# Optimization experiments

Measured on AMD Instinct MI355X. Metric: run time of the kernel, lower is better.

The kernel has to match this reference:

```python
import jax, jax.numpy as jnp
import numpy as np

N_EMBD = 1024
N_HEAD = 16
HEAD_DIM = N_EMBD // N_HEAD


def setup_inputs() -> dict:
    key = jax.random.key(0)
    ks = jax.random.split(key, 9)
    B, S = 4, 2048
    s = 1.0 / np.sqrt(N_EMBD)
    return {
        "x": jax.random.normal(ks[0], (B, S, N_EMBD), dtype=jnp.float32),
        "attention_mask": jnp.ones((B, S), dtype=jnp.int32),
        "Wq": jax.random.normal(ks[1], (N_EMBD, N_EMBD), jnp.float32) * s,
        "bq": jnp.zeros((N_EMBD,), jnp.float32),
        "Wk": jax.random.normal(ks[2], (N_EMBD, N_EMBD), jnp.float32) * s,
        "bk": jnp.zeros((N_EMBD,), jnp.float32),
        "Wv": jax.random.normal(ks[3], (N_EMBD, N_EMBD), jnp.float32) * s,
        "bv": jnp.zeros((N_EMBD,), jnp.float32),
        "Wo": jax.random.normal(ks[4], (N_EMBD, N_EMBD), jnp.float32) * s,
        "bo": jnp.zeros((N_EMBD,), jnp.float32),
    }


def _split_heads(t):  # [B,S,E] -> [B,H,S,D]
    B, S, _ = t.shape
    return t.reshape(B, S, N_HEAD, HEAD_DIM).transpose(0, 2, 1, 3)


def reference(x, attention_mask, Wq, bq, Wk, bk, Wv, bv, Wo, bo):
    B, S, E = x.shape
    q = _split_heads(x @ Wq.T + bq)
    k = _split_heads(x @ Wk.T + bk)
    v = _split_heads(x @ Wv.T + bv)
    # scores: [B,H,S,S]
    scores = jnp.einsum('bhqd,bhkd->bhqk', q, k) / np.sqrt(HEAD_DIM).astype(np.float32)
    # additive mask: 0 where mask==1, -inf where mask==0, broadcast over heads/query
    mask = jnp.where(attention_mask[:, None, None, :] == 0, -jnp.inf, 0.0).astype(scores.dtype)
    scores = scores + mask
    probs = jax.nn.softmax(scores, axis=-1)  # dropout p=0 -> identity
    ctx = jnp.einsum('bhqk,bhkd->bhqd', probs, v)
    out = ctx.transpose(0, 2, 1, 3).reshape(B, S, E)
    return out @ Wo.T + bo
```

## Files before the change

### kernel.cpp

```cpp
#include <hip/hip_runtime.h>

typedef __bf16 bf16;
typedef __attribute__((ext_vector_type(2))) bf16 bf16x2;
typedef __attribute__((ext_vector_type(4))) bf16 bf16x4;
typedef __attribute__((ext_vector_type(8))) bf16 bf16x8;
typedef __attribute__((ext_vector_type(4))) float f32x4;
typedef __attribute__((ext_vector_type(16))) float f32x16;
typedef __attribute__((ext_vector_type(4))) int i32x4;
typedef __attribute__((ext_vector_type(2))) int i32x2;

#define MFMA_BF16(a, b, c) __builtin_amdgcn_mfma_f32_16x16x32_bf16((a), (b), (c), 0, 0, 0)
#define MFMA32(a, b, c)    __builtin_amdgcn_mfma_f32_32x32x16_bf16((a), (b), (c), 0, 0, 0)

constexpr int S_LEN = 2048;
constexpr int EMB   = 1024;
constexpr int NHEAD = 16;
constexpr int HDIM  = 64;
constexpr int BATCH = 4;
constexpr int NTOK  = BATCH * S_LEN;

__device__ __forceinline__ void gload_lds16(const bf16* g, bf16* l) {
    __builtin_amdgcn_global_load_lds(
        (const __attribute__((address_space(1))) void*)g,
        (__attribute__((address_space(3))) void*)l, 16, 0, 0);
}

__device__ __forceinline__ int pkbf(float a, float b) {
    bf16x2 t; t[0] = (bf16)a; t[1] = (bf16)b;
    return __builtin_bit_cast(int, t);
}

#if __has_builtin(__builtin_amdgcn_permlane32_swap)
__device__ __forceinline__ i32x2 permswap(int a, int b) {
    return __builtin_amdgcn_permlane32_swap(a, b, false, false);
}
#else
__device__ __forceinline__ i32x2 permswap(int a, int b) {
    int as = __shfl_xor(a, 32);
    int bs = __shfl_xor(b, 32);
    int hx_ = (threadIdx.x >> 5) & 1;
    i32x2 r;
    r[0] = hx_ ? bs : a;
    r[1] = hx_ ? b : as;
    return r;
}
#endif

__global__ __launch_bounds__(256)
void cvt_f32_bf16(const float* __restrict__ src, bf16* __restrict__ dst, int n4) {
    int i = blockIdx.x * 256 + threadIdx.x;
    if (i < n4) {
        f32x4 v = ((const f32x4*)src)[i];
        bf16x4 o;
        o[0] = (bf16)v[0]; o[1] = (bf16)v[1]; o[2] = (bf16)v[2]; o[3] = (bf16)v[3];
        ((bf16x4*)dst)[i] = o;
    }
}

__global__ __launch_bounds__(256)
void gemm_bt(const bf16* __restrict__ A,
             const bf16* __restrict__ W0, const bf16* __restrict__ W1, const bf16* __restrict__ W2,
             const float* __restrict__ b0, const float* __restrict__ b1, const float* __restrict__ b2,
             void* __restrict__ d0, void* __restrict__ d1, void* __restrict__ d2,
             int fused, float q_scale)
{
    __shared__ bf16 al[128 * 32];
    __shared__ bf16 bl[128 * 32];

    int seg, mode, n0;
    if (fused) { seg = blockIdx.y >> 3; n0 = (blockIdx.y & 7) * 128; mode = (seg == 2) ? 1 : 0; }
    else       { seg = 0;              n0 = blockIdx.y * 128;        mode = 2; }
    const bf16*  W    = seg == 0 ? W0 : (seg == 1 ? W1 : W2);
    const float* bias = seg == 0 ? b0 : (seg == 1 ? b1 : b2);
    void*        C    = seg == 0 ? d0 : (seg == 1 ? d1 : d2);
    const float  osc  = (fused && seg == 0) ? q_scale : 1.0f;

    const int tid  = threadIdx.x;
    const int lane = tid & 63;
    const int w    = tid >> 6;
    const int quad = lane >> 4;
    const int l16  = lane & 15;
    const int wm   = (w >> 1) * 64;
    const int wn   = (w & 1) * 64;
    const int m0   = blockIdx.x * 128;

    f32x4 acc[4][4] = {};

    for (int k0 = 0; k0 < EMB; k0 += 32) {
        #pragma unroll
        for (int c = 0; c < 2; ++c) {
            int idx = c * 256 + tid;
            int row = idx >> 2, kc = idx & 3;
            gload_lds16(A + (size_t)(m0 + row) * EMB + k0 + kc * 8, &al[idx * 8]);
            gload_lds16(W + (size_t)(n0 + row) * EMB + k0 + kc * 8, &bl[idx * 8]);
        }
        __syncthreads();

        bf16x8 afrag[4], bfrag[4];
        #pragma unroll
        for (int t = 0; t < 4; ++t)
            afrag[t] = *(const bf16x8*)&al[(wm + t * 16 + l16) * 32 + quad * 8];
        #pragma unroll
        for (int t = 0; t < 4; ++t)
            bfrag[t] = *(const bf16x8*)&bl[(wn + t * 16 + l16) * 32 + quad * 8];

        #pragma unroll
        for (int mt = 0; mt < 4; ++mt)
            #pragma unroll
            for (int nt = 0; nt < 4; ++nt)
                acc[mt][nt] = MFMA_BF16(afrag[mt], bfrag[nt], acc[mt][nt]);

        __syncthreads();
    }

    #pragma unroll
    for (int mt = 0; mt < 4; ++mt) {
        #pragma unroll
        for (int nt = 0; nt < 4; ++nt) {
            int col = n0 + wn + nt * 16 + l16;
            float bv = bias[col];
            int row0 = m0 + wm + mt * 16 + quad * 4;
            if (mode == 1) {
                int bb = row0 >> 11, s0 = row0 & 2047;
                int hh = col >> 6,   d  = col & 63;
                bf16x4 pk;
                #pragma unroll
                for (int r = 0; r < 4; ++r) pk[r] = (bf16)(acc[mt][nt][r] + bv);
                *(bf16x4*)((bf16*)C + (size_t)((bb * NHEAD + hh) * HDIM + d) * S_LEN + s0) = pk;
            } else if (mode == 0) {
                #pragma unroll
                for (int r = 0; r < 4; ++r)
                    ((bf16*)C)[(size_t)(row0 + r) * EMB + col] = (bf16)((acc[mt][nt][r] + bv) * osc);
            } else {
                #pragma unroll
                for (int r = 0; r < 4; ++r)
                    ((float*)C)[(size_t)(row0 + r) * EMB + col] = acc[mt][nt][r] + bv;
            }
        }
    }
}

__global__ __launch_bounds__(512)
void flash_attn(const bf16* __restrict__ qg, const bf16* __restrict__ kg,
                const bf16* __restrict__ vtg, const int* __restrict__ maskg,
                bf16* __restrict__ ctx)
{
    __shared__ bf16  klds[2][64 * 64];
    __shared__ bf16  vlds[2][64 * 64];
    __shared__ bf16  bias_lds[2048];
    __shared__ float stat_lds[8][32];

    const int fb  = blockIdx.x;
    const int xcd = fb & 7;
    const int rr  = fb >> 3;
    const int qi  = rr & 7;
    const int gg  = rr >> 3;
    const int g   = gg * 8 + xcd;
    const int h   = g & 15;
    const int b   = g >> 4;
    const int q0  = qi * 256;

    const int tid  = threadIdx.x;
    const int lane = tid & 63;
    const int w    = tid >> 6;
    const int l32  = lane & 31;
    const int hx   = lane >> 5;

    const int srow  = tid >> 3;
    const int sslot = (tid & 7) ^ (srow & 7);

    int ok;
    {
        int i = tid * 4;
        i32x4 mv = *(const i32x4*)(maskg + b * S_LEN + i);
        bf16x4 bb;
        ok = 1;
        #pragma unroll
        for (int r = 0; r < 4; ++r) {
            ok &= (mv[r] != 0);
            bb[r] = mv[r] ? (bf16)0.f : (bf16)(-3.0e38f);
        }
        *(bf16x4*)&bias_lds[i] = bb;
    }
    const int allvalid = __syncthreads_and(ok);

    bf16x8 qf[4];
    {
        const bf16* qrow = qg + (size_t)(b * S_LEN + q0 + w * 32 + l32) * EMB + h * HDIM + hx * 8;
        qf[0] = *(const bf16x8*)(qrow);
        qf[1] = *(const bf16x8*)(qrow + 16);
        qf[2] = *(const bf16x8*)(qrow + 32);
        qf[3] = *(const bf16x8*)(qrow + 48);
    }

    const bf16* kgb = kg  + (size_t)b * S_LEN * EMB + h * HDIM;
    const bf16* vgb = vtg + (size_t)((b * NHEAD + h) * HDIM) * S_LEN;

    float mrow = -1e30f, lpart = 0.f;
    f32x16 o0, o1;
    #pragma unroll
    for (int r = 0; r < 16; ++r) { o0[r] = 0.f; o1[r] = 0.f; }

#define STAGE(BUF, KT) {                                                            \
    gload_lds16(kgb + (size_t)((KT) * 64 + srow) * EMB + sslot * 8,                 \
                &klds[BUF][tid * 8]);                                               \
    gload_lds16(vgb + (size_t)srow * S_LEN + (KT) * 64 + sslot * 8,                 \
                &vlds[BUF][tid * 8]);                                               \
}

#define LDSK(CUR, ROW, SB) (*(const bf16x8*)((const char*)&klds[CUR][0] + ((ROW) << 7) + ((((SB) ^ ((ROW) & 7))) << 4)))
#define LDSV(CUR, ROW, SB) (*(const bf16x8*)((const char*)&vlds[CUR][0] + ((ROW) << 7) + ((((SB) ^ ((ROW) & 7))) << 4)))

#define SUBTILE(CUR, KT, KK) {                                                      \
    f32x16 s_;                                                                      \
    _Pragma("unroll") for (int r_ = 0; r_ < 16; ++r_) s_[r_] = 0.f;                 \
    const int krow_ = (KK) * 32 + l32;                                              \
    __builtin_amdgcn_s_setprio(1);                                                  \
    s_ = MFMA32(LDSK(CUR, krow_, 0 * 2 + hx), qf[0], s_);                           \
    s_ = MFMA32(LDSK(CUR, krow_, 1 * 2 + hx), qf[1], s_);                           \
    s_ = MFMA32(LDSK(CUR, krow_, 2 * 2 + hx), qf[2], s_);                           \
    s_ = MFMA32(LDSK(CUR, krow_, 3 * 2 + hx), qf[3], s_);                           \
    __builtin_amdgcn_s_setprio(0);                                                  \
    if (!allvalid) {                                                                \
        _Pragma("unroll") for (int s4_ = 0; s4_ < 4; ++s4_) {                       \
            bf16x4 b4_ = *(const bf16x4*)&bias_lds[(KT) * 64 + (KK) * 32 + s4_ * 8 + hx * 4]; \
            _Pragma("unroll") for (int t_ = 0; t_ < 4; ++t_)                        \
                s_[4 * s4_ + t_] += (float)b4_[t_];                                 \
        }                                                                           \
    }                                                                               \
    float rmax_ = s_[0];                                                            \
    _Pragma("unroll") for (int r_ = 1; r_ < 16; ++r_) rmax_ = fmaxf(rmax_, s_[r_]); \
    rmax_ = fmaxf(rmax_, __shfl_xor(rmax_, 32));                                    \
    if (!__all(rmax_ <= mrow + 8.f)) {                                              \
        float mnew_  = fmaxf(mrow, rmax_);                                          \
        float alpha_ = __builtin_amdgcn_exp2f(mrow - mnew_);                        \
        mrow = mnew_; lpart *= alpha_;                                              \
        if (hx == 0) stat_lds[w][l32] = alpha_;                                     \
        _Pragma("unroll") for (int s4_ = 0; s4_ < 4; ++s4_) {                       \
            f32x4 a4_ = *(const f32x4*)&stat_lds[w][s4_ * 8 + hx * 4];              \
            _Pragma("unroll") for (int t_ = 0; t_ < 4; ++t_) {                      \
                o0[4 * s4_ + t_] *= a4_[t_]; o1[4 * s4_ + t_] *= a4_[t_];           \
            }                                                                       \
        }                                                                           \
    }                                                                               \
    bf16x8 pa0, pa1;                                                                \
    {                                                                               \
        float p_[8];                                                                \
        _Pragma("unroll") for (int r_ = 0; r_ < 8; ++r_) {                          \
            p_[r_] = __builtin_amdgcn_exp2f(s_[r_] - mrow); lpart += p_[r_];        \
        }                                                                           \
        i32x2 r0_ = permswap(pkbf(p_[0], p_[1]), pkbf(p_[4], p_[5]));               \
        i32x2 r1_ = permswap(pkbf(p_[2], p_[3]), pkbf(p_[6], p_[7]));               \
        i32x4 fw_; fw_[0] = r0_[0]; fw_[1] = r1_[0]; fw_[2] = r0_[1]; fw_[3] = r1_[1]; \
        pa0 = __builtin_bit_cast(bf16x8, fw_);                                      \
    }                                                                               \
    {                                                                               \
        float p_[8];                                                                \
        _Pragma("unroll") for (int r_ = 0; r_ < 8; ++r_) {                          \
            p_[r_] = __builtin_amdgcn_exp2f(s_[8 + r_] - mrow); lpart += p_[r_];    \
        }                                                                           \
        i32x2 r0_ = permswap(pkbf(p_[0], p_[1]), pkbf(p_[4], p_[5]));               \
        i32x2 r1_ = permswap(pkbf(p_[2], p_[3]), pkbf(p_[6], p_[7]));               \
        i32x4 fw_; fw_[0] = r0_[0]; fw_[1] = r1_[0]; fw_[2] = r0_[1]; fw_[3] = r1_[1]; \
        pa1 = __builtin_bit_cast(bf16x8, fw_);                                      \
    }                                                                               \
    __builtin_amdgcn_s_setprio(1);                                                  \
    o0 = MFMA32(pa0, LDSV(CUR, 0 * 32 + l32, (KK) * 4 + 0 * 2 + hx), o0);           \
    o1 = MFMA32(pa0, LDSV(CUR, 1 * 32 + l32, (KK) * 4 + 0 * 2 + hx), o1);           \
    o0 = MFMA32(pa1, LDSV(CUR, 0 * 32 + l32, (KK) * 4 + 1 * 2 + hx), o0);           \
    o1 = MFMA32(pa1, LDSV(CUR, 1 * 32 + l32, (KK) * 4 + 1 * 2 + hx), o1);           \
    __builtin_amdgcn_s_setprio(0);                                                  \
}

    STAGE(0, 0)
    __syncthreads();

    for (int kt = 0; kt < 32; ++kt) {
        const int cur = kt & 1;
        if (kt + 1 < 32) STAGE(cur ^ 1, kt + 1)
        SUBTILE(cur, kt, 0)
        SUBTILE(cur, kt, 1)
        __syncthreads();
    }

#undef SUBTILE
#undef LDSK
#undef LDSV
#undef STAGE

    float lrow = lpart + __shfl_xor(lpart, 32);
    float inv  = lrow > 0.f ? 1.f / lrow : 0.f;
    if (hx == 0) stat_lds[w][l32] = inv;
    #pragma unroll
    for (int s4 = 0; s4 < 4; ++s4) {
        f32x4 i4 = *(const f32x4*)&stat_lds[w][s4 * 8 + hx * 4];
        #pragma unroll
        for (int t = 0; t < 4; ++t) {
            size_t row = (size_t)(b * S_LEN + q0 + w * 32 + s4 * 8 + hx * 4 + t);
            bf16* cp = ctx + row * EMB + h * HDIM + l32;
            cp[0]  = (bf16)(o0[4 * s4 + t] * i4[t]);
            cp[32] = (bf16)(o1[4 * s4 + t] * i4[t]);
        }
    }
}

extern "C" void kernel_launch(void* const* d_in, const int* in_sizes, int n_in,
                              void* d_out, int out_size, void* d_ws, size_t ws_size,
                              hipStream_t stream)
{
    const float* x   = (const float*)d_in[0];
    const int*  mask = (const int*)d_in[1];
    const float* Wq  = (const float*)d_in[2];
    const float* bq  = (const float*)d_in[3];
    const float* Wk  = (const float*)d_in[4];
    const float* bk  = (const float*)d_in[5];
    const float* Wv  = (const float*)d_in[6];
    const float* bv  = (const float*)d_in[7];
    const float* Wo  = (const float*)d_in[8];
    const float* bo  = (const float*)d_in[9];
    (void)in_sizes; (void)n_in; (void)out_size; (void)ws_size;

    const size_t me = (size_t)NTOK * EMB;
    const size_t we = (size_t)EMB * EMB;
    bf16* xb  = (bf16*)d_ws;
    bf16* qb  = xb  + me;
    bf16* kb  = qb  + me;
    bf16* vt  = kb  + me;
    bf16* wqb = vt  + me;
    bf16* wkb = wqb + we;
    bf16* wvb = wkb + we;
    bf16* wob = wvb + we;
    bf16* cx  = xb;

    cvt_f32_bf16<<<(int)(me / 4 / 256), 256, 0, stream>>>(x,  xb,  (int)(me / 4));
    cvt_f32_bf16<<<(int)(we / 4 / 256), 256, 0, stream>>>(Wq, wqb, (int)(we / 4));
    cvt_f32_bf16<<<(int)(we / 4 / 256), 256, 0, stream>>>(Wk, wkb, (int)(we / 4));
    cvt_f32_bf16<<<(int)(we / 4 / 256), 256, 0, stream>>>(Wv, wvb, (int)(we / 4));
    cvt_f32_bf16<<<(int)(we / 4 / 256), 256, 0, stream>>>(Wo, wob, (int)(we / 4));

    gemm_bt<<<dim3(NTOK / 128, 24), 256, 0, stream>>>(
        xb, wqb, wkb, wvb, bq, bk, bv, qb, kb, vt, 1, 0.18033688011112042f);

    flash_attn<<<dim3(512), 512, 0, stream>>>(qb, kb, vt, mask, cx);

    gemm_bt<<<dim3(NTOK / 128, EMB / 128), 256, 0, stream>>>(
        cx, wob, wob, wob, bo, bo, bo, d_out, d_out, d_out, 0, 1.0f);
}
```

Measured before the change: 282.7 us.

## Replace GEMM with 256x256 double-buffered pipelined kernel and merge weight conversions

Replaces the 128x128 single-buffered GEMM with a 256x256-tile, 512-thread kernel. It double-buffers K-chunks of 64 in LDS, prefetches the next chunk with global_load_lds while MFMAs run, XOR-swizzles LDS rows to avoid bank conflicts, and raises MFMA priority with s_setprio. The four weight-conversion launches are merged into one kernel, cutting launch overhead. Larger tiles raise arithmetic intensity but halve the grid: the output projection gets only 128 blocks on a 256-CU part, and the QKV projection 384.

```diff
diff --git a/kernel.cpp b/kernel.cpp
--- a/kernel.cpp
+++ b/kernel.cpp
@@ -58,18 +58,30 @@
 }
 
 __global__ __launch_bounds__(256)
-void gemm_bt(const bf16* __restrict__ A,
+void cvt_w4(const float* __restrict__ s0, const float* __restrict__ s1,
+            const float* __restrict__ s2, const float* __restrict__ s3,
+            bf16* __restrict__ dst) {
+    const int a = blockIdx.y;
+    const float* s = a == 0 ? s0 : (a == 1 ? s1 : (a == 2 ? s2 : s3));
+    int i = blockIdx.x * 256 + threadIdx.x;
+    f32x4 v = ((const f32x4*)s)[i];
+    bf16x4 o;
+    o[0] = (bf16)v[0]; o[1] = (bf16)v[1]; o[2] = (bf16)v[2]; o[3] = (bf16)v[3];
+    ((bf16x4*)(dst + (size_t)a * EMB * EMB))[i] = o;
+}
+
+__global__ __launch_bounds__(512)
+void gemm256(const bf16* __restrict__ A,
              const bf16* __restrict__ W0, const bf16* __restrict__ W1, const bf16* __restrict__ W2,
              const float* __restrict__ b0, const float* __restrict__ b1, const float* __restrict__ b2,
              void* __restrict__ d0, void* __restrict__ d1, void* __restrict__ d2,
              int fused, float q_scale)
 {
-    __shared__ bf16 al[128 * 32];
-    __shared__ bf16 bl[128 * 32];
+    __shared__ bf16 lds[2][4][8192];
 
     int seg, mode, n0;
-    if (fused) { seg = blockIdx.y >> 3; n0 = (blockIdx.y & 7) * 128; mode = (seg == 2) ? 1 : 0; }
-    else       { seg = 0;              n0 = blockIdx.y * 128;        mode = 2; }
+    if (fused) { seg = blockIdx.y >> 2; n0 = (blockIdx.y & 3) * 256; mode = (seg == 2) ? 1 : 0; }
+    else       { seg = 0;              n0 = blockIdx.y * 256;        mode = 2; }
     const bf16*  W    = seg == 0 ? W0 : (seg == 1 ? W1 : W2);
     const float* bias = seg == 0 ? b0 : (seg == 1 ? b1 : b2);
     void*        C    = seg == 0 ? d0 : (seg == 1 ? d1 : d2);
@@ -78,63 +90,117 @@
     const int tid  = threadIdx.x;
     const int lane = tid & 63;
     const int w    = tid >> 6;
+    const int wr   = w >> 2;
+    const int wc   = w & 3;
     const int quad = lane >> 4;
     const int l16  = lane & 15;
-    const int wm   = (w >> 1) * 64;
-    const int wn   = (w & 1) * 64;
-    const int m0   = blockIdx.x * 128;
-
-    f32x4 acc[4][4] = {};
-
-    for (int k0 = 0; k0 < EMB; k0 += 32) {
+    const int m0   = blockIdx.x * 256;
+
+#define STAGE_A(BUF, H, T) {                                                        \
+    _Pragma("unroll") for (int c_ = 0; c_ < 2; ++c_) {                              \
+        int idx_ = c_ * 512 + tid;                                                  \
+        int m_ = idx_ >> 2, s_ = idx_ & 3;                                          \
+        gload_lds16(A + (size_t)(m0 + m_) * EMB + (T) * 64 + (H) * 32               \
+                      + ((s_ ^ ((m_ >> 1) & 3)) << 3),                              \
+                    &lds[BUF][H][idx_ * 8]);                                        \
+    } }
+#define STAGE_B(BUF, H, T) {                                                        \
+    _Pragma("unroll") for (int c_ = 0; c_ < 2; ++c_) {                              \
+        int idx_ = c_ * 512 + tid;                                                  \
+        int n_ = idx_ >> 2, s_ = idx_ & 3;                                          \
+        gload_lds16(W + (size_t)(n0 + n_) * EMB + (T) * 64 + (H) * 32               \
+                      + ((s_ ^ ((n_ >> 1) & 3)) << 3),                              \
+                    &lds[BUF][2 + (H)][idx_ * 8]);                                  \
+    } }
+
+#define READ_A(DST, BUF, H, G) {                                                    \
+    _Pragma("unroll") for (int i_ = 0; i_ < 4; ++i_) {                              \
+        int m_ = wr * 128 + (G) * 64 + i_ * 16 + l16;                               \
+        DST[i_] = *(const bf16x8*)&lds[BUF][H][m_ * 32 + ((quad ^ ((m_ >> 1) & 3)) << 3)]; \
+    } }
+#define READ_B(DST, BUF, H) {                                                       \
+    _Pragma("unroll") for (int j_ = 0; j_ < 4; ++j_) {                              \
+        int n_ = wc * 64 + j_ * 16 + l16;                                           \
+        DST[j_] = *(const bf16x8*)&lds[BUF][2 + (H)][n_ * 32 + ((quad ^ ((n_ >> 1) & 3)) << 3)]; \
+    } }
+
+#define MFMA_PH(AF, BF, G) {                                                        \
+    __builtin_amdgcn_s_setprio(1);                                                  \
+    _Pragma("unroll") for (int i_ = 0; i_ < 4; ++i_)                                \
+        _Pragma("unroll") for (int j_ = 0; j_ < 4; ++j_)                            \
+            acc[(G) * 4 + i_][j_] = MFMA_BF16(AF[i_], BF[j_], acc[(G) * 4 + i_][j_]); \
+    __builtin_amdgcn_s_setprio(0);                                                  \
+}
+
+    f32x4 acc[8][4] = {};
+
+    STAGE_A(0, 0, 0) STAGE_B(0, 0, 0) STAGE_A(0, 1, 0) STAGE_B(0, 1, 0)
+    asm volatile("s_waitcnt vmcnt(4)" ::: "memory");
+    __builtin_amdgcn_s_barrier();
+    __builtin_amdgcn_sched_barrier(0);
+
+    for (int t = 0; t < 16; ++t) {
+        const int cur  = t & 1;
+        const int nxt  = cur ^ 1;
+        const bool more = (t + 1 < 16);
+        bf16x8 afr[4], bfr[4];
+
+        READ_B(bfr, cur, 0)
+        READ_A(afr, cur, 0, 0)
+        if (more) STAGE_A(nxt, 0, t + 1)
+        MFMA_PH(afr, bfr, 0)
+
+        READ_A(afr, cur, 0, 1)
+        if (more) STAGE_B(nxt, 0, t + 1)
+        MFMA_PH(afr, bfr, 1)
+        if (more) asm volatile("s_waitcnt vmcnt(4)" ::: "memory");
+        else      asm volatile("s_waitcnt vmcnt(0)" ::: "memory");
+        __builtin_amdgcn_s_barrier();
+        __builtin_amdgcn_sched_barrier(0);
+
+        READ_B(bfr, cur, 1)
+        READ_A(afr, cur, 1, 0)
+        if (more) STAGE_A(nxt, 1, t + 1)
+        MFMA_PH(afr, bfr, 0)
+
+        READ_A(afr, cur, 1, 1)
+        if (more) STAGE_B(nxt, 1, t + 1)
+        MFMA_PH(afr, bfr, 1)
+        if (more) {
+            asm volatile("s_waitcnt vmcnt(4)" ::: "memory");
+            __builtin_amdgcn_s_barrier();
+            __builtin_amdgcn_sched_barrier(0);
+        }
+    }
+
+#undef STAGE_A
+#undef STAGE_B
+#undef READ_A
+#undef READ_B
+#undef MFMA_PH
+
+    #pragma unroll
+    for (int ii = 0; ii < 8; ++ii) {
         #pragma unroll
-        for (int c = 0; c < 2; ++c) {
-            int idx = c * 256 + tid;
-            int row = idx >> 2, kc = idx & 3;
-            gload_lds16(A + (size_t)(m0 + row) * EMB + k0 + kc * 8, &al[idx * 8]);
-            gload_lds16(W + (size_t)(n0 + row) * EMB + k0 + kc * 8, &bl[idx * 8]);
-        }
-        __syncthreads();
-
-        bf16x8 afrag[4], bfrag[4];
-        #pragma unroll
-        for (int t = 0; t < 4; ++t)
-            afrag[t] = *(const bf16x8*)&al[(wm + t * 16 + l16) * 32 + quad * 8];
-        #pragma unroll
-        for (int t = 0; t < 4; ++t)
-            bfrag[t] = *(const bf16x8*)&bl[(wn + t * 16 + l16) * 32 + quad * 8];
-
-        #pragma unroll
-        for (int mt = 0; mt < 4; ++mt)
-            #pragma unroll
-            for (int nt = 0; nt < 4; ++nt)
-                acc[mt][nt] = MFMA_BF16(afrag[mt], bfrag[nt], acc[mt][nt]);
-
-        __syncthreads();
-    }
-
-    #pragma unroll
-    for (int mt = 0; mt < 4; ++mt) {
-        #pragma unroll
-        for (int nt = 0; nt < 4; ++nt) {
-            int col = n0 + wn + nt * 16 + l16;
+        for (int j = 0; j < 4; ++j) {
+            int col = n0 + wc * 64 + j * 16 + l16;
             float bv = bias[col];
-            int row0 = m0 + wm + mt * 16 + quad * 4;
+            int row0 = m0 + wr * 128 + ii * 16 + quad * 4;
             if (mode == 1) {
                 int bb = row0 >> 11, s0 = row0 & 2047;
                 int hh = col >> 6,   d  = col & 63;
                 bf16x4 pk;
                 #pragma unroll
-                for (int r = 0; r < 4; ++r) pk[r] = (bf16)(acc[mt][nt][r] + bv);
+                for (int r = 0; r < 4; ++r) pk[r] = (bf16)(acc[ii][j][r] + bv);
                 *(bf16x4*)((bf16*)C + (size_t)((bb * NHEAD + hh) * HDIM + d) * S_LEN + s0) = pk;
             } else if (mode == 0) {
                 #pragma unroll
                 for (int r = 0; r < 4; ++r)
-                    ((bf16*)C)[(size_t)(row0 + r) * EMB + col] = (bf16)((acc[mt][nt][r] + bv) * osc);
+                    ((bf16*)C)[(size_t)(row0 + r) * EMB + col] = (bf16)((acc[ii][j][r] + bv) * osc);
             } else {
                 #pragma unroll
                 for (int r = 0; r < 4; ++r)
-                    ((float*)C)[(size_t)(row0 + r) * EMB + col] = acc[mt][nt][r] + bv;
+                    ((float*)C)[(size_t)(row0 + r) * EMB + col] = acc[ii][j][r] + bv;
             }
         }
     }
@@ -332,17 +398,14 @@
     bf16* wob = wvb + we;
     bf16* cx  = xb;
 
-    cvt_f32_bf16<<<(int)(me / 4 / 256), 256, 0, stream>>>(x,  xb,  (int)(me / 4));
-    cvt_f32_bf16<<<(int)(we / 4 / 256), 256, 0, stream>>>(Wq, wqb, (int)(we / 4));
-    cvt_f32_bf16<<<(int)(we / 4 / 256), 256, 0, stream>>>(Wk, wkb, (int)(we / 4));
-    cvt_f32_bf16<<<(int)(we / 4 / 256), 256, 0, stream>>>(Wv, wvb, (int)(we / 4));
-    cvt_f32_bf16<<<(int)(we / 4 / 256), 256, 0, stream>>>(Wo, wob, (int)(we / 4));
-
-    gemm_bt<<<dim3(NTOK / 128, 24), 256, 0, stream>>>(
+    cvt_f32_bf16<<<(int)(me / 4 / 256), 256, 0, stream>>>(x, xb, (int)(me / 4));
+    cvt_w4<<<dim3((int)(we / 4 / 256), 4), 256, 0, stream>>>(Wq, Wk, Wv, Wo, wqb);
+
+    gemm256<<<dim3(NTOK / 256, 12), 512, 0, stream>>>(
         xb, wqb, wkb, wvb, bq, bk, bv, qb, kb, vt, 1, 0.18033688011112042f);
 
     flash_attn<<<dim3(512), 512, 0, stream>>>(qb, kb, vt, mask, cx);
 
-    gemm_bt<<<dim3(NTOK / 128, EMB / 128), 256, 0, stream>>>(
+    gemm256<<<dim3(NTOK / 256, EMB / 256), 512, 0, stream>>>(
         cx, wob, wob, wob, bo, bo, bo, d_out, d_out, d_out, 0, 1.0f);
 }
```

Measured after the change: 285.7 us. Within noise of the previous version (+1.1%).
